# Kernel optimization log

Hardware: AMD Instinct MI355X
Metric: run time of the kernel (lower is better)

Reference implementation:

```python
import jax, jax.numpy as jnp
import numpy as np

B, S, D, H = 8, 1024, 1024, 16
HD = D // H  # head dim 64

def setup_inputs() -> dict:
    key = jax.random.key(0)
    ks = jax.random.split(key, 7)
    def w(k):
        return jax.random.normal(k, (D, D), dtype=jnp.float32) * (1.0 / np.sqrt(D))
    return {
        'q': jax.random.normal(ks[0], (B, S, D), dtype=jnp.float32),
        'k': jax.random.normal(ks[1], (B, S, D), dtype=jnp.float32),
        'v': jax.random.normal(ks[2], (B, S, D), dtype=jnp.float32),
        'Wq': w(ks[3]), 'Wk': w(ks[4]), 'Wv': w(ks[5]), 'Wo': w(ks[6]),
    }

def reference(q, k, v, Wq, Wk, Wv, Wo):
    # projections (nn.Linear, no bias): y = x @ W.T
    def heads(x, W):
        return (x @ W.T).reshape(B, S, H, HD)
    qh, kh, vh = heads(q, Wq), heads(k, Wk), heads(v, Wv)
    scale = 1.0 / np.sqrt(HD).astype(np.float32)
    scores = jnp.einsum('bqhd,bkhd->bhqk', qh, kh) * scale  # [B,H,S,S]
    # masked=True -> causal mask
    causal = jnp.tril(jnp.ones((S, S), dtype=bool))
    scores = jnp.where(causal[None, None], scores, jnp.float32(-1e9))
    attn = jax.nn.softmax(scores, axis=-1)
    out = jnp.einsum('bhqk,bkhd->bqhd', attn, vh).reshape(B, S, D)
    return out @ Wo.T
```

## Files before the change

### kernel.cpp

```cpp
#include <hip/hip_runtime.h>
#include <hip/hip_bf16.h>

#define B_ 8
#define S_ 1024
#define D_ 1024
#define H_ 16
#define HD_ 64
#define M_ (B_*S_)
#define NQB (S_/128)

typedef __attribute__((ext_vector_type(8))) short short8;
typedef __attribute__((ext_vector_type(4))) short short4v;
typedef __attribute__((ext_vector_type(4))) float f32x4;
typedef __attribute__((ext_vector_type(16))) float f32x16;
typedef __attribute__((ext_vector_type(4))) int int4v;
typedef __attribute__((ext_vector_type(2))) int int2v;

#define CSC 0.18033688f

__device__ __forceinline__ unsigned short f2bf(float f) {
    unsigned int u = __float_as_uint(f);
    u += 0x7FFF + ((u >> 16) & 1);
    return (unsigned short)(u >> 16);
}

__device__ __forceinline__ void gload16(const void* g, void* l) {
    __builtin_amdgcn_global_load_lds(
        (const __attribute__((address_space(1))) void*)g,
        (__attribute__((address_space(3))) void*)l, 16, 0, 0);
}

__device__ __forceinline__ int2v plswap(int a, int b) {
    return __builtin_amdgcn_permlane32_swap(a, b, false, false);
}

__device__ __forceinline__ float max3f(float a, float b, float c) {
    return fmaxf(fmaxf(a, b), c);
}

struct CvtSeg { const float* src; unsigned short* dst; };
struct CvtArgs { CvtSeg s[4]; };

__global__ __launch_bounds__(256)
void cvt_w(CvtArgs a)
{
    const CvtSeg seg = a.s[blockIdx.y];
    int i = blockIdx.x * 256 + threadIdx.x;
    float4 x = reinterpret_cast<const float4*>(seg.src)[i*2];
    float4 y = reinterpret_cast<const float4*>(seg.src)[i*2+1];
    short8 v = short8{(short)f2bf(x.x),(short)f2bf(x.y),(short)f2bf(x.z),(short)f2bf(x.w),
                      (short)f2bf(y.x),(short)f2bf(y.y),(short)f2bf(y.z),(short)f2bf(y.w)};
    reinterpret_cast<short8*>(seg.dst)[i] = v;
}

__device__ __forceinline__ void gemm_core_f32A(
    const float* __restrict__ A, const unsigned short* __restrict__ Wb,
    short* lds, int m0, int n0, int tid, f32x4 (&acc)[4][4])
{
    const int K = D_;
    const int lane = tid & 63, wave = tid >> 6;
    const int wr = wave >> 1, wc = wave & 1;
    const int r16 = lane & 15, g4 = lane >> 4;
    const int sr8  = lane >> 3;
    const int slot = lane & 7;
    const int scol = ((lane ^ sr8) & 7) * 8;
    const int wsl  = (slot ^ sr8) << 3;

    float4 ar0[4][2], ar1[4][2];

    #define STAGEB(t, bi)                                                     \
        { _Pragma("unroll")                                                   \
          for (int c = 0; c < 4; ++c) {                                       \
              int chunk = wave*4 + c;                                         \
              gload16(Wb + (size_t)(n0 + chunk*8 + sr8) * K + (t)*64 + scol,  \
                      lds + (bi)*16384 + 8192 + chunk*512);                   \
          } }

    #define LOADA_S(t, AR)                                                    \
        { _Pragma("unroll")                                                   \
          for (int c = 0; c < 4; ++c) {                                       \
              const float* src = A + (size_t)(m0 + wave*32 + c*8 + sr8)*K     \
                                   + (t)*64 + slot*8;                         \
              AR[c][0] = *reinterpret_cast<const float4*>(src);               \
              AR[c][1] = *reinterpret_cast<const float4*>(src + 4);           \
          } }

    #define WRITEA_S(bi, AR)                                                  \
        { _Pragma("unroll")                                                   \
          for (int c = 0; c < 4; ++c) {                                       \
              unsigned w0, w1, w2, w3;                                        \
              asm("v_cvt_pk_bf16_f32 %0, %1, %2" : "=v"(w0) : "v"(AR[c][0].x), "v"(AR[c][0].y)); \
              asm("v_cvt_pk_bf16_f32 %0, %1, %2" : "=v"(w1) : "v"(AR[c][0].z), "v"(AR[c][0].w)); \
              asm("v_cvt_pk_bf16_f32 %0, %1, %2" : "=v"(w2) : "v"(AR[c][1].x), "v"(AR[c][1].y)); \
              asm("v_cvt_pk_bf16_f32 %0, %1, %2" : "=v"(w3) : "v"(AR[c][1].z), "v"(AR[c][1].w)); \
              int4v wi; wi.x = (int)w0; wi.y = (int)w1; wi.z = (int)w2; wi.w = (int)w3; \
              *reinterpret_cast<int4v*>(                                      \
                  &lds[(bi)*16384 + (wave*32 + c*8 + sr8)*64 + wsl]) = wi;    \
          } }

    const int NT = K / 64;

    STAGEB(0, 0);
    LOADA_S(0, ar0);
    asm volatile("s_waitcnt vmcnt(0)" ::: "memory");
    WRITEA_S(0, ar0);
    LOADA_S(1, ar1);
    asm volatile("s_waitcnt lgkmcnt(0)" ::: "memory");
    __builtin_amdgcn_s_barrier();

    #define ITER(t, cur, ARCUR, AROTH)                                        \
    {                                                                         \
        if ((t) + 1 < NT) STAGEB((t)+1, (cur)^1);                             \
        if ((t) + 2 < NT) LOADA_S((t)+2, ARCUR);                              \
        const short* Ab = lds + (cur)*16384;                                  \
        const short* Bb = Ab + 8192;                                          \
        _Pragma("unroll")                                                     \
        for (int ks = 0; ks < 2; ++ks) {                                      \
            short8 af[4], bf[4];                                              \
            _Pragma("unroll")                                                 \
            for (int m = 0; m < 4; ++m) {                                     \
                int r = wr*64 + m*16 + r16;                                   \
                af[m] = *reinterpret_cast<const short8*>(                     \
                    &Ab[r*64 + (((ks*4 + g4) ^ (r16 & 7)) << 3)]);            \
            }                                                                 \
            _Pragma("unroll")                                                 \
            for (int n = 0; n < 4; ++n) {                                     \
                int r = wc*64 + n*16 + r16;                                   \
                bf[n] = *reinterpret_cast<const short8*>(                     \
                    &Bb[r*64 + (((ks*4 + g4) ^ (r16 & 7)) << 3)]);            \
            }                                                                 \
            __builtin_amdgcn_s_setprio(1);                                    \
            _Pragma("unroll")                                                 \
            for (int m = 0; m < 4; ++m)                                       \
                _Pragma("unroll")                                             \
                for (int n = 0; n < 4; ++n)                                   \
                    acc[m][n] = __builtin_amdgcn_mfma_f32_16x16x32_bf16(af[m], bf[n], acc[m][n], 0, 0, 0); \
            __builtin_amdgcn_s_setprio(0);                                    \
        }                                                                     \
        if ((t) + 1 < NT) {                                                   \
            if ((t) + 2 < NT) asm volatile("s_waitcnt vmcnt(8)" ::: "memory");\
            else              asm volatile("s_waitcnt vmcnt(0)" ::: "memory");\
            WRITEA_S((cur)^1, AROTH);                                         \
            asm volatile("s_waitcnt lgkmcnt(0)" ::: "memory");                \
        }                                                                     \
        __builtin_amdgcn_s_barrier();                                         \
    }

    for (int t = 0; t < NT; t += 2) {
        ITER(t,     0, ar0, ar1);
        ITER(t + 1, 1, ar1, ar0);
    }
    #undef ITER
    #undef STAGEB
    #undef LOADA_S
    #undef WRITEA_S
}

__device__ __forceinline__ void gemm_core_bf16A(
    const unsigned short* __restrict__ A, const unsigned short* __restrict__ Wb,
    short* lds, int m0, int n0, int tid, f32x4 (&acc)[4][4])
{
    const int K = D_;
    const int lane = tid & 63, wave = tid >> 6;
    const int wr = wave >> 1, wc = wave & 1;
    const int r16 = lane & 15, g4 = lane >> 4;
    const int srow = lane >> 3;
    const int scol = ((lane ^ srow) & 7) * 8;

    #define STAGE(t, bi)                                                      \
        { _Pragma("unroll")                                                   \
          for (int c = 0; c < 4; ++c) {                                       \
              int chunk = wave*4 + c;                                         \
              gload16(Wb + (size_t)(n0 + chunk*8 + srow) * K + (t)*64 + scol, \
                      lds + (bi)*16384 + 8192 + chunk*512);                   \
              gload16(A + (size_t)(m0 + chunk*8 + srow) * K + (t)*64 + scol,  \
                      lds + (bi)*16384 + chunk*512);                          \
          } }

    STAGE(0, 0);

    const int NT = K / 64;
    for (int t = 0; t < NT; ++t) {
        const int cur = t & 1;
        if (t + 1 < NT) {
            STAGE(t+1, cur^1);
            asm volatile("s_waitcnt vmcnt(8)" ::: "memory");
        } else {
            asm volatile("s_waitcnt vmcnt(0)" ::: "memory");
        }
        __builtin_amdgcn_s_barrier();

        const short* Ab = lds + cur*16384;
        const short* Bb = Ab + 8192;
        #pragma unroll
        for (int ks = 0; ks < 2; ++ks) {
            short8 af[4], bf[4];
            #pragma unroll
            for (int m = 0; m < 4; ++m) {
                int r = wr*64 + m*16 + r16;
                af[m] = *reinterpret_cast<const short8*>(
                    &Ab[r*64 + (((ks*4 + g4) ^ (r16 & 7)) << 3)]);
            }
            #pragma unroll
            for (int n = 0; n < 4; ++n) {
                int r = wc*64 + n*16 + r16;
                bf[n] = *reinterpret_cast<const short8*>(
                    &Bb[r*64 + (((ks*4 + g4) ^ (r16 & 7)) << 3)]);
            }
            __builtin_amdgcn_s_setprio(1);
            #pragma unroll
            for (int m = 0; m < 4; ++m)
                #pragma unroll
                for (int n = 0; n < 4; ++n)
                    acc[m][n] = __builtin_amdgcn_mfma_f32_16x16x32_bf16(af[m], bf[n], acc[m][n], 0, 0, 0);
            __builtin_amdgcn_s_setprio(0);
        }
        __builtin_amdgcn_s_barrier();
    }
    #undef STAGE
}

template<int MODE>
__device__ __forceinline__ void epilogue_vec(
    float* Cl, void* __restrict__ Ov, int m0, int n0, int tid, f32x4 (&acc)[4][4])
{
    const int N = D_;
    const int lane = tid & 63, wave = tid >> 6;
    const int wr = wave >> 1, wc = wave & 1;
    const int r16 = lane & 15, g4 = lane >> 4;

    #pragma unroll
    for (int p = 0; p < 2; ++p) {
        if (p) __syncthreads();
        if (wr == p) {
            #pragma unroll
            for (int m = 0; m < 4; ++m)
                #pragma unroll
                for (int n = 0; n < 4; ++n)
                    #pragma unroll
                    for (int i = 0; i < 4; ++i)
                        Cl[(m*16 + g4*4 + i)*132 + wc*64 + n*16 + r16] = acc[m][n][i];
        }
        __syncthreads();
        if (MODE == 1) {
            #pragma unroll
            for (int j = 0; j < 8; ++j) {
                int c = j*256 + tid;
                int row = c >> 5, cg = c & 31;
                float4 val = *reinterpret_cast<const float4*>(&Cl[row*132 + cg*4]);
                *reinterpret_cast<float4*>(
                    &((float*)Ov)[(size_t)(m0 + p*64 + row)*N + n0 + cg*4]) = val;
            }
        } else {
            #pragma unroll
            for (int j = 0; j < 4; ++j) {
                int c2 = j*256 + tid;
                int row = c2 >> 4, col = (c2 & 15)*8;
                float4 a = *reinterpret_cast<const float4*>(&Cl[row*132 + col]);
                float4 bq = *reinterpret_cast<const float4*>(&Cl[row*132 + col + 4]);
                if (MODE == 3) {
                    a.x *= CSC; a.y *= CSC; a.z *= CSC; a.w *= CSC;
                    bq.x *= CSC; bq.y *= CSC; bq.z *= CSC; bq.w *= CSC;
                }
                short8 v = short8{(short)f2bf(a.x),(short)f2bf(a.y),(short)f2bf(a.z),(short)f2bf(a.w),
                                  (short)f2bf(bq.x),(short)f2bf(bq.y),(short)f2bf(bq.z),(short)f2bf(bq.w)};
                *reinterpret_cast<short8*>(
                    &((unsigned short*)Ov)[(size_t)(m0 + p*64 + row)*N + n0 + col]) = v;
            }
        }
    }
}

struct ProjArgs {
    const float* A[3];
    const unsigned short* W[3];
    void* O[3];
};

__global__ __launch_bounds__(256)
void gemm_proj(ProjArgs pa)
{
    __shared__ __align__(16) short lds[32768];

    const int L = blockIdx.x;
    const int which = L >> 9;
    const int inner = L & 511;
    const int xcd = inner & 7, jj = inner >> 3;
    const int m0 = (xcd*8 + (jj >> 3)) * 128;
    const int n0 = (jj & 7) * 128;
    const int tid = threadIdx.x;

    f32x4 acc[4][4] = {};
    gemm_core_f32A(pa.A[which], pa.W[which], lds, m0, n0, tid, acc);

    if (which == 2) {
        const int lane = tid & 63, wave = tid >> 6;
        const int wr = wave >> 1, wc = wave & 1;
        const int r16 = lane & 15, g4 = lane >> 4;
        #pragma unroll
        for (int m = 0; m < 4; ++m) {
            int row0 = m0 + wr*64 + m*16 + g4*4;
            #pragma unroll
            for (int n = 0; n < 4; ++n) {
                int col = n0 + wc*64 + n*16 + r16;
                size_t vrow = (size_t)((row0 >> 10)*16 + (col >> 6))*64 + (col & 63);
                short4v pk = short4v{(short)f2bf(acc[m][n][0]), (short)f2bf(acc[m][n][1]),
                                     (short)f2bf(acc[m][n][2]), (short)f2bf(acc[m][n][3])};
                *reinterpret_cast<short4v*>((unsigned short*)pa.O[2] + vrow*S_ + (row0 & 1023)) = pk;
            }
        }
    } else if (which == 0) {
        epilogue_vec<3>((float*)lds, pa.O[0], m0, n0, tid, acc);
    } else {
        epilogue_vec<0>((float*)lds, pa.O[1], m0, n0, tid, acc);
    }
}

__global__ __launch_bounds__(256)
void gemm_final(const unsigned short* __restrict__ A, const unsigned short* __restrict__ Wb,
                float* __restrict__ Ov)
{
    __shared__ __align__(16) short lds[32768];

    const int L = blockIdx.x;
    const int xcd = L & 7, jj = L >> 3;
    const int m0 = (xcd*8 + (jj >> 3)) * 128;
    const int n0 = (jj & 7) * 128;
    const int tid = threadIdx.x;

    f32x4 acc[4][4] = {};
    gemm_core_bf16A(A, Wb, lds, m0, n0, tid, acc);
    epilogue_vec<1>((float*)lds, Ov, m0, n0, tid, acc);
}

__global__ __launch_bounds__(256)
void attn_fwd(const unsigned short* __restrict__ Qh,
              const unsigned short* __restrict__ Kh,
              const unsigned short* __restrict__ VtG,
              unsigned short* __restrict__ AO)
{
    __shared__ __align__(16) short Kl[2][64*64];
    __shared__ __align__(16) short Vl[2][64*64];

    const int tid  = threadIdx.x;
    const int lane = tid & 63, wave = tid >> 6;
    const int l31 = lane & 31, h32 = lane >> 5;
    const int L = blockIdx.x;
    const int xcd = L & 7, jj = L >> 3;
    const int pr = jj & 3;
    const int hb = xcd*16 + (jj >> 2);
    const int h = hb & 15, b = hb >> 4;

    const int slot = tid & 7;
    const int r0 = tid >> 3, r1 = r0 + 32;
    const int koff0 = r0*64 + ((slot ^ (r0 & 7)) << 3);
    const int koff1 = r1*64 + ((slot ^ (r1 & 7)) << 3);

    const unsigned short* Kg0 = Kh + ((size_t)b*S_)*D_ + h*HD_;
    const unsigned short* Vg0 = VtG + ((size_t)(b*H_ + h)*HD_)*S_;

    for (int t = 0; t < 2; ++t) {
        const int qb = t ? pr : (NQB - 1 - pr);
        const int q0w = qb*128 + wave*32;
        const int qi  = q0w + l31;

        short8 qf[4];
        #pragma unroll
        for (int m = 0; m < 4; ++m)
            qf[m] = *reinterpret_cast<const short8*>(
                Qh + ((size_t)b*S_ + qi)*D_ + h*HD_ + m*16 + h32*8);

        f32x16 o0 = {}, o1 = {};
        float mrow = -1e30f, lsum = 0.f;
        const int nkb = 2*qb + 2;

        short8 ka, kc, va, vc;
        ka = *reinterpret_cast<const short8*>(Kg0 + (size_t)r0*D_ + slot*8);
        kc = *reinterpret_cast<const short8*>(Kg0 + (size_t)r1*D_ + slot*8);
        va = *reinterpret_cast<const short8*>(Vg0 + (size_t)r0*S_ + slot*8);
        vc = *reinterpret_cast<const short8*>(Vg0 + (size_t)r1*S_ + slot*8);
        *reinterpret_cast<short8*>(&Kl[0][koff0]) = ka;
        *reinterpret_cast<short8*>(&Kl[0][koff1]) = kc;
        *reinterpret_cast<short8*>(&Vl[0][koff0]) = va;
        *reinterpret_cast<short8*>(&Vl[0][koff1]) = vc;
        __syncthreads();

        for (int kb = 0; kb < nkb; ++kb) {
            const int cur = kb & 1;
            const bool havenext = (kb + 1 < nkb);
            if (havenext) {
                const unsigned short* Kg = Kg0 + (size_t)(kb+1)*64*D_;
                const unsigned short* Vg = Vg0 + (kb+1)*64;
                ka = *reinterpret_cast<const short8*>(Kg + (size_t)r0*D_ + slot*8);
                kc = *reinterpret_cast<const short8*>(Kg + (size_t)r1*D_ + slot*8);
                va = *reinterpret_cast<const short8*>(Vg + (size_t)r0*S_ + slot*8);
                vc = *reinterpret_cast<const short8*>(Vg + (size_t)r1*S_ + slot*8);
            }

            if (kb*64 <= q0w + 31) {
                f32x16 p0 = {}, p1 = {};
                __builtin_amdgcn_s_setprio(1);
                #pragma unroll
                for (int m = 0; m < 4; ++m) {
                    short8 kf0 = *reinterpret_cast<const short8*>(
                        &Kl[cur][l31*64 + ((((m<<1)|h32) ^ (l31 & 7)) << 3)]);
                    short8 kf1 = *reinterpret_cast<const short8*>(
                        &Kl[cur][(32 + l31)*64 + ((((m<<1)|h32) ^ (l31 & 7)) << 3)]);
                    p0 = __builtin_amdgcn_mfma_f32_32x32x16_bf16(kf0, qf[m], p0, 0, 0, 0);
                    p1 = __builtin_amdgcn_mfma_f32_32x32x16_bf16(kf1, qf[m], p1, 0, 0, 0);
                }
                __builtin_amdgcn_s_setprio(0);

                if (kb*64 + 63 > q0w) {
                    #pragma unroll
                    for (int r = 0; r < 16; ++r) {
                        int kk = (r & 3) + ((r >> 2) << 3) + (h32 << 2);
                        if (kb*64      + kk > qi) p0[r] = -1e30f;
                        if (kb*64 + 32 + kk > qi) p1[r] = -1e30f;
                    }
                }

                float t0 = max3f(p0[0],  p0[1],  p0[2]);
                float t1 = max3f(p0[3],  p0[4],  p0[5]);
                float t2 = max3f(p0[6],  p0[7],  p0[8]);
                float t3 = max3f(p0[9],  p0[10], p0[11]);
                float t4 = max3f(p0[12], p0[13], p0[14]);
                float t5 = max3f(p0[15], p1[0],  p1[1]);
                float t6 = max3f(p1[2],  p1[3],  p1[4]);
                float t7 = max3f(p1[5],  p1[6],  p1[7]);
                float t8 = max3f(p1[8],  p1[9],  p1[10]);
                float t9 = max3f(p1[11], p1[12], p1[13]);
                float ta = fmaxf(p1[14], p1[15]);
                float mloc = fmaxf(max3f(max3f(t0,t1,t2), max3f(t3,t4,t5), max3f(t6,t7,t8)),
                                   fmaxf(t9, ta));
                int2v mm = plswap(__float_as_int(mloc), __float_as_int(mloc));
                float pm = fmaxf(__int_as_float(mm.x), __int_as_float(mm.y));

                if (__any(pm > mrow + 11.5416f)) {
                    float mn = fmaxf(mrow, pm);
                    float so = exp2f(mrow - mn);
                    #pragma unroll
                    for (int r = 0; r < 16; ++r) { o0[r] *= so; o1[r] *= so; }
                    lsum *= so;
                    mrow = mn;
                }

                #pragma unroll
                for (int r = 0; r < 16; ++r) p0[r] = exp2f(p0[r] - mrow);
                #pragma unroll
                for (int r = 0; r < 16; ++r) p1[r] = exp2f(p1[r] - mrow);
                float sq[8];
                #pragma unroll
                for (int r = 0; r < 8; ++r)
                    sq[r] = (p0[2*r] + p0[2*r+1]) + (p1[2*r] + p1[2*r+1]);
                float rs = ((sq[0]+sq[1]) + (sq[2]+sq[3])) + ((sq[4]+sq[5]) + (sq[6]+sq[7]));
                int2v ss = plswap(__float_as_int(rs), __float_as_int(rs));
                lsum += __int_as_float(ss.x) + __int_as_float(ss.y);

                #pragma unroll
                for (int m = 0; m < 4; ++m) {
                    const int mb = (m & 1) * 8;
                    unsigned int C0, C1, C2, C3;
                    if (m < 2) {
                        asm("v_cvt_pk_bf16_f32 %0, %1, %2" : "=v"(C0) : "v"(p0[mb+0]), "v"(p0[mb+1]));
                        asm("v_cvt_pk_bf16_f32 %0, %1, %2" : "=v"(C1) : "v"(p0[mb+2]), "v"(p0[mb+3]));
                        asm("v_cvt_pk_bf16_f32 %0, %1, %2" : "=v"(C2) : "v"(p0[mb+4]), "v"(p0[mb+5]));
                        asm("v_cvt_pk_bf16_f32 %0, %1, %2" : "=v"(C3) : "v"(p0[mb+6]), "v"(p0[mb+7]));
                    } else {
                        asm("v_cvt_pk_bf16_f32 %0, %1, %2" : "=v"(C0) : "v"(p1[mb+0]), "v"(p1[mb+1]));
                        asm("v_cvt_pk_bf16_f32 %0, %1, %2" : "=v"(C1) : "v"(p1[mb+2]), "v"(p1[mb+3]));
                        asm("v_cvt_pk_bf16_f32 %0, %1, %2" : "=v"(C2) : "v"(p1[mb+4]), "v"(p1[mb+5]));
                        asm("v_cvt_pk_bf16_f32 %0, %1, %2" : "=v"(C3) : "v"(p1[mb+6]), "v"(p1[mb+7]));
                    }
                    int2v s0 = plswap((int)C0, (int)C2);
                    int2v s1 = plswap((int)C1, (int)C3);
                    int4v wi; wi.x = s0.x; wi.y = s1.x; wi.z = s0.y; wi.w = s1.y;
                    short8 pf = __builtin_bit_cast(short8, wi);

                    short8 vf0 = *reinterpret_cast<const short8*>(
                        &Vl[cur][l31*64 + ((((m<<1)|h32) ^ (l31 & 7)) << 3)]);
                    short8 vf1 = *reinterpret_cast<const short8*>(
                        &Vl[cur][(32 + l31)*64 + ((((m<<1)|h32) ^ (l31 & 7)) << 3)]);
                    o0 = __builtin_amdgcn_mfma_f32_32x32x16_bf16(vf0, pf, o0, 0, 0, 0);
                    o1 = __builtin_amdgcn_mfma_f32_32x32x16_bf16(vf1, pf, o1, 0, 0, 0);
                }
            }

            if (havenext) {
                const int nb = cur ^ 1;
                *reinterpret_cast<short8*>(&Kl[nb][koff0]) = ka;
                *reinterpret_cast<short8*>(&Kl[nb][koff1]) = kc;
                *reinterpret_cast<short8*>(&Vl[nb][koff0]) = va;
                *reinterpret_cast<short8*>(&Vl[nb][koff1]) = vc;
            }
            __syncthreads();
        }

        float inv = 1.f / lsum;
        #pragma unroll
        for (int tt = 0; tt < 2; ++tt) {
            #pragma unroll
            for (int g = 0; g < 4; ++g) {
                short4v pk;
                #pragma unroll
                for (int j = 0; j < 4; ++j) {
                    float val = (tt ? o1[g*4+j] : o0[g*4+j]) * inv;
                    pk[j] = (short)f2bf(val);
                }
                int d = tt*32 + g*8 + h32*4;
                *reinterpret_cast<short4v*>(AO + ((size_t)b*S_ + qi)*D_ + h*HD_ + d) = pk;
            }
        }
    }
}

extern "C" void kernel_launch(void* const* d_in, const int* in_sizes, int n_in,
                              void* d_out, int out_size, void* d_ws, size_t ws_size,
                              hipStream_t stream) {
    const float* q  = (const float*)d_in[0];
    const float* k  = (const float*)d_in[1];
    const float* v  = (const float*)d_in[2];
    const float* Wq = (const float*)d_in[3];
    const float* Wk = (const float*)d_in[4];
    const float* Wv = (const float*)d_in[5];
    const float* Wo = (const float*)d_in[6];

    unsigned short* Wqb = (unsigned short*)d_ws;
    unsigned short* Wkb = Wqb + (size_t)D_*D_;
    unsigned short* Wvb = Wkb + (size_t)D_*D_;
    unsigned short* Wob = Wvb + (size_t)D_*D_;
    unsigned short* Qh  = Wob + (size_t)D_*D_;
    unsigned short* Kh  = Qh  + (size_t)M_*D_;
    unsigned short* VtG = Kh  + (size_t)M_*D_;
    unsigned short* AO  = VtG + (size_t)M_*D_;

    dim3 blk(256);
    CvtArgs ca;
    ca.s[0] = CvtSeg{Wq, Wqb};
    ca.s[1] = CvtSeg{Wk, Wkb};
    ca.s[2] = CvtSeg{Wv, Wvb};
    ca.s[3] = CvtSeg{Wo, Wob};
    cvt_w<<<dim3(512, 4), blk, 0, stream>>>(ca);

    ProjArgs pa;
    pa.A[0] = q;  pa.W[0] = Wqb; pa.O[0] = Qh;
    pa.A[1] = k;  pa.W[1] = Wkb; pa.O[1] = Kh;
    pa.A[2] = v;  pa.W[2] = Wvb; pa.O[2] = VtG;
    gemm_proj<<<dim3(1536), blk, 0, stream>>>(pa);

    attn_fwd<<<dim3(512), blk, 0, stream>>>(Qh, Kh, VtG, AO);

    gemm_final<<<dim3(512), blk, 0, stream>>>(AO, Wob, (float*)d_out);
}
```

Measured before the change: 151.5 us.

## Stage 128-key K/V tiles via direct global-to-LDS loads in attention

The attention loop now processes 128 keys per iteration as two 64-key halves, with double-buffered LDS holding 128-row K and V tiles. The tiles are filled by asynchronous global-to-LDS loads (gload16). The XOR swizzle moves to the global source column, so the LDS destinations stay linear. This halves the number of barrier and stage cycles, removes the register round trip for staging, and issues both QK^T MMA groups back to back before softmax. In exchange, LDS per block doubles to 64KB, which may cut occupancy. An explicit vmcnt(0) wait before each barrier also limits how much load latency is hidden.

```diff
diff --git a/kernel.cpp b/kernel.cpp
--- a/kernel.cpp
+++ b/kernel.cpp
@@ -339,8 +339,8 @@
               const unsigned short* __restrict__ VtG,
               unsigned short* __restrict__ AO)
 {
-    __shared__ __align__(16) short Kl[2][64*64];
-    __shared__ __align__(16) short Vl[2][64*64];
+    __shared__ __align__(16) short Kl[2][2][64*64];
+    __shared__ __align__(16) short Vl[2][2][64*64];
 
     const int tid  = threadIdx.x;
     const int lane = tid & 63, wave = tid >> 6;
@@ -353,11 +353,108 @@
 
     const int slot = tid & 7;
     const int r0 = tid >> 3, r1 = r0 + 32;
-    const int koff0 = r0*64 + ((slot ^ (r0 & 7)) << 3);
-    const int koff1 = r1*64 + ((slot ^ (r1 & 7)) << 3);
+    const int sc8 = ((slot ^ (r0 & 7)) << 3);
 
     const unsigned short* Kg0 = Kh + ((size_t)b*S_)*D_ + h*HD_;
     const unsigned short* Vg0 = VtG + ((size_t)(b*H_ + h)*HD_)*S_;
+
+    #define STAGEKV128(j1, nb)                                                \
+        { const unsigned short* Kg = Kg0 + (size_t)(j1)*128*D_;               \
+          const unsigned short* Vg = Vg0 + (size_t)(j1)*128;                  \
+          gload16(Kg + (size_t)r0*D_ + sc8,      &Kl[nb][0][r0*64 + slot*8]); \
+          gload16(Kg + (size_t)r1*D_ + sc8,      &Kl[nb][0][r1*64 + slot*8]); \
+          gload16(Kg + (size_t)(r0+64)*D_ + sc8, &Kl[nb][1][r0*64 + slot*8]); \
+          gload16(Kg + (size_t)(r1+64)*D_ + sc8, &Kl[nb][1][r1*64 + slot*8]); \
+          gload16(Vg + (size_t)r0*S_ + sc8,      &Vl[nb][0][r0*64 + slot*8]); \
+          gload16(Vg + (size_t)r1*S_ + sc8,      &Vl[nb][0][r1*64 + slot*8]); \
+          gload16(Vg + 64 + (size_t)r0*S_ + sc8, &Vl[nb][1][r0*64 + slot*8]); \
+          gload16(Vg + 64 + (size_t)r1*S_ + sc8, &Vl[nb][1][r1*64 + slot*8]); }
+
+    #define QKT_W(cur, vw, p0, p1)                                            \
+        { __builtin_amdgcn_s_setprio(1);                                      \
+          _Pragma("unroll")                                                   \
+          for (int m = 0; m < 4; ++m) {                                       \
+              short8 kf0 = *reinterpret_cast<const short8*>(                  \
+                  &Kl[cur][vw][l31*64 + ((((m<<1)|h32) ^ (l31 & 7)) << 3)]);  \
+              short8 kf1 = *reinterpret_cast<const short8*>(                  \
+                  &Kl[cur][vw][(32 + l31)*64 + ((((m<<1)|h32) ^ (l31 & 7)) << 3)]); \
+              p0 = __builtin_amdgcn_mfma_f32_32x32x16_bf16(kf0, qf[m], p0, 0, 0, 0); \
+              p1 = __builtin_amdgcn_mfma_f32_32x32x16_bf16(kf1, qf[m], p1, 0, 0, 0); \
+          }                                                                   \
+          __builtin_amdgcn_s_setprio(0); }
+
+    #define MASK_W(kb, p0, p1)                                                \
+        if ((kb)*64 + 63 > q0w) {                                             \
+            _Pragma("unroll")                                                 \
+            for (int r = 0; r < 16; ++r) {                                    \
+                int kk = (r & 3) + ((r >> 2) << 3) + (h32 << 2);              \
+                if ((kb)*64      + kk > qi) p0[r] = -1e30f;                   \
+                if ((kb)*64 + 32 + kk > qi) p1[r] = -1e30f;                   \
+            } }
+
+    #define SOFTMAX_W(p0, p1) {                                               \
+        float t0 = max3f(p0[0],  p0[1],  p0[2]);                              \
+        float t1 = max3f(p0[3],  p0[4],  p0[5]);                              \
+        float t2 = max3f(p0[6],  p0[7],  p0[8]);                              \
+        float t3 = max3f(p0[9],  p0[10], p0[11]);                             \
+        float t4 = max3f(p0[12], p0[13], p0[14]);                             \
+        float t5 = max3f(p0[15], p1[0],  p1[1]);                              \
+        float t6 = max3f(p1[2],  p1[3],  p1[4]);                              \
+        float t7 = max3f(p1[5],  p1[6],  p1[7]);                              \
+        float t8 = max3f(p1[8],  p1[9],  p1[10]);                             \
+        float t9 = max3f(p1[11], p1[12], p1[13]);                             \
+        float ta = fmaxf(p1[14], p1[15]);                                     \
+        float mloc = fmaxf(max3f(max3f(t0,t1,t2), max3f(t3,t4,t5),            \
+                                 max3f(t6,t7,t8)), fmaxf(t9, ta));            \
+        int2v mm = plswap(__float_as_int(mloc), __float_as_int(mloc));        \
+        float pm = fmaxf(__int_as_float(mm.x), __int_as_float(mm.y));         \
+        if (__any(pm > mrow + 11.5416f)) {                                    \
+            float mn = fmaxf(mrow, pm);                                       \
+            float so = exp2f(mrow - mn);                                      \
+            _Pragma("unroll")                                                 \
+            for (int r = 0; r < 16; ++r) { o0[r] *= so; o1[r] *= so; }        \
+            lsum *= so;                                                       \
+            mrow = mn;                                                        \
+        }                                                                     \
+        _Pragma("unroll")                                                     \
+        for (int r = 0; r < 16; ++r) p0[r] = exp2f(p0[r] - mrow);             \
+        _Pragma("unroll")                                                     \
+        for (int r = 0; r < 16; ++r) p1[r] = exp2f(p1[r] - mrow);             \
+        float sq[8];                                                          \
+        _Pragma("unroll")                                                     \
+        for (int r = 0; r < 8; ++r)                                           \
+            sq[r] = (p0[2*r] + p0[2*r+1]) + (p1[2*r] + p1[2*r+1]);            \
+        float rs = ((sq[0]+sq[1]) + (sq[2]+sq[3])) + ((sq[4]+sq[5]) + (sq[6]+sq[7])); \
+        int2v ss = plswap(__float_as_int(rs), __float_as_int(rs));            \
+        lsum += __int_as_float(ss.x) + __int_as_float(ss.y); }
+
+    #define PV_W(cur, vw, p0, p1)                                             \
+        { _Pragma("unroll")                                                   \
+          for (int m = 0; m < 4; ++m) {                                       \
+              const int mb = (m & 1) * 8;                                     \
+              unsigned int C0, C1, C2, C3;                                    \
+              if (m < 2) {                                                    \
+                  asm("v_cvt_pk_bf16_f32 %0, %1, %2" : "=v"(C0) : "v"(p0[mb+0]), "v"(p0[mb+1])); \
+                  asm("v_cvt_pk_bf16_f32 %0, %1, %2" : "=v"(C1) : "v"(p0[mb+2]), "v"(p0[mb+3])); \
+                  asm("v_cvt_pk_bf16_f32 %0, %1, %2" : "=v"(C2) : "v"(p0[mb+4]), "v"(p0[mb+5])); \
+                  asm("v_cvt_pk_bf16_f32 %0, %1, %2" : "=v"(C3) : "v"(p0[mb+6]), "v"(p0[mb+7])); \
+              } else {                                                        \
+                  asm("v_cvt_pk_bf16_f32 %0, %1, %2" : "=v"(C0) : "v"(p1[mb+0]), "v"(p1[mb+1])); \
+                  asm("v_cvt_pk_bf16_f32 %0, %1, %2" : "=v"(C1) : "v"(p1[mb+2]), "v"(p1[mb+3])); \
+                  asm("v_cvt_pk_bf16_f32 %0, %1, %2" : "=v"(C2) : "v"(p1[mb+4]), "v"(p1[mb+5])); \
+                  asm("v_cvt_pk_bf16_f32 %0, %1, %2" : "=v"(C3) : "v"(p1[mb+6]), "v"(p1[mb+7])); \
+              }                                                               \
+              int2v s0 = plswap((int)C0, (int)C2);                            \
+              int2v s1 = plswap((int)C1, (int)C3);                            \
+              int4v wi; wi.x = s0.x; wi.y = s1.x; wi.z = s0.y; wi.w = s1.y;   \
+              short8 pf = __builtin_bit_cast(short8, wi);                     \
+              short8 vf0 = *reinterpret_cast<const short8*>(                  \
+                  &Vl[cur][vw][l31*64 + ((((m<<1)|h32) ^ (l31 & 7)) << 3)]);  \
+              short8 vf1 = *reinterpret_cast<const short8*>(                  \
+                  &Vl[cur][vw][(32 + l31)*64 + ((((m<<1)|h32) ^ (l31 & 7)) << 3)]); \
+              o0 = __builtin_amdgcn_mfma_f32_32x32x16_bf16(vf0, pf, o0, 0, 0, 0); \
+              o1 = __builtin_amdgcn_mfma_f32_32x32x16_bf16(vf1, pf, o1, 0, 0, 0); \
+          } }
 
     for (int t = 0; t < 2; ++t) {
         const int qb = t ? pr : (NQB - 1 - pr);
@@ -372,127 +469,34 @@
 
         f32x16 o0 = {}, o1 = {};
         float mrow = -1e30f, lsum = 0.f;
-        const int nkb = 2*qb + 2;
-
-        short8 ka, kc, va, vc;
-        ka = *reinterpret_cast<const short8*>(Kg0 + (size_t)r0*D_ + slot*8);
-        kc = *reinterpret_cast<const short8*>(Kg0 + (size_t)r1*D_ + slot*8);
-        va = *reinterpret_cast<const short8*>(Vg0 + (size_t)r0*S_ + slot*8);
-        vc = *reinterpret_cast<const short8*>(Vg0 + (size_t)r1*S_ + slot*8);
-        *reinterpret_cast<short8*>(&Kl[0][koff0]) = ka;
-        *reinterpret_cast<short8*>(&Kl[0][koff1]) = kc;
-        *reinterpret_cast<short8*>(&Vl[0][koff0]) = va;
-        *reinterpret_cast<short8*>(&Vl[0][koff1]) = vc;
+        const int np = qb + 1;
+
+        STAGEKV128(0, 0);
+        asm volatile("s_waitcnt vmcnt(0)" ::: "memory");
         __syncthreads();
 
-        for (int kb = 0; kb < nkb; ++kb) {
-            const int cur = kb & 1;
-            const bool havenext = (kb + 1 < nkb);
-            if (havenext) {
-                const unsigned short* Kg = Kg0 + (size_t)(kb+1)*64*D_;
-                const unsigned short* Vg = Vg0 + (kb+1)*64;
-                ka = *reinterpret_cast<const short8*>(Kg + (size_t)r0*D_ + slot*8);
-                kc = *reinterpret_cast<const short8*>(Kg + (size_t)r1*D_ + slot*8);
-                va = *reinterpret_cast<const short8*>(Vg + (size_t)r0*S_ + slot*8);
-                vc = *reinterpret_cast<const short8*>(Vg + (size_t)r1*S_ + slot*8);
-            }
-
-            if (kb*64 <= q0w + 31) {
-                f32x16 p0 = {}, p1 = {};
-                __builtin_amdgcn_s_setprio(1);
-                #pragma unroll
-                for (int m = 0; m < 4; ++m) {
-                    short8 kf0 = *reinterpret_cast<const short8*>(
-                        &Kl[cur][l31*64 + ((((m<<1)|h32) ^ (l31 & 7)) << 3)]);
-                    short8 kf1 = *reinterpret_cast<const short8*>(
-                        &Kl[cur][(32 + l31)*64 + ((((m<<1)|h32) ^ (l31 & 7)) << 3)]);
-                    p0 = __builtin_amdgcn_mfma_f32_32x32x16_bf16(kf0, qf[m], p0, 0, 0, 0);
-                    p1 = __builtin_amdgcn_mfma_f32_32x32x16_bf16(kf1, qf[m], p1, 0, 0, 0);
-                }
-                __builtin_amdgcn_s_setprio(0);
-
-                if (kb*64 + 63 > q0w) {
-                    #pragma unroll
-                    for (int r = 0; r < 16; ++r) {
-                        int kk = (r & 3) + ((r >> 2) << 3) + (h32 << 2);
-                        if (kb*64      + kk > qi) p0[r] = -1e30f;
-                        if (kb*64 + 32 + kk > qi) p1[r] = -1e30f;
-                    }
-                }
-
-                float t0 = max3f(p0[0],  p0[1],  p0[2]);
-                float t1 = max3f(p0[3],  p0[4],  p0[5]);
-                float t2 = max3f(p0[6],  p0[7],  p0[8]);
-                float t3 = max3f(p0[9],  p0[10], p0[11]);
-                float t4 = max3f(p0[12], p0[13], p0[14]);
-                float t5 = max3f(p0[15], p1[0],  p1[1]);
-                float t6 = max3f(p1[2],  p1[3],  p1[4]);
-                float t7 = max3f(p1[5],  p1[6],  p1[7]);
-                float t8 = max3f(p1[8],  p1[9],  p1[10]);
-                float t9 = max3f(p1[11], p1[12], p1[13]);
-                float ta = fmaxf(p1[14], p1[15]);
-                float mloc = fmaxf(max3f(max3f(t0,t1,t2), max3f(t3,t4,t5), max3f(t6,t7,t8)),
-                                   fmaxf(t9, ta));
-                int2v mm = plswap(__float_as_int(mloc), __float_as_int(mloc));
-                float pm = fmaxf(__int_as_float(mm.x), __int_as_float(mm.y));
-
-                if (__any(pm > mrow + 11.5416f)) {
-                    float mn = fmaxf(mrow, pm);
-                    float so = exp2f(mrow - mn);
-                    #pragma unroll
-                    for (int r = 0; r < 16; ++r) { o0[r] *= so; o1[r] *= so; }
-                    lsum *= so;
-                    mrow = mn;
-                }
-
-                #pragma unroll
-                for (int r = 0; r < 16; ++r) p0[r] = exp2f(p0[r] - mrow);
-                #pragma unroll
-                for (int r = 0; r < 16; ++r) p1[r] = exp2f(p1[r] - mrow);
-                float sq[8];
-                #pragma unroll
-                for (int r = 0; r < 8; ++r)
-                    sq[r] = (p0[2*r] + p0[2*r+1]) + (p1[2*r] + p1[2*r+1]);
-                float rs = ((sq[0]+sq[1]) + (sq[2]+sq[3])) + ((sq[4]+sq[5]) + (sq[6]+sq[7]));
-                int2v ss = plswap(__float_as_int(rs), __float_as_int(rs));
-                lsum += __int_as_float(ss.x) + __int_as_float(ss.y);
-
-                #pragma unroll
-                for (int m = 0; m < 4; ++m) {
-                    const int mb = (m & 1) * 8;
-                    unsigned int C0, C1, C2, C3;
-                    if (m < 2) {
-                        asm("v_cvt_pk_bf16_f32 %0, %1, %2" : "=v"(C0) : "v"(p0[mb+0]), "v"(p0[mb+1]));
-                        asm("v_cvt_pk_bf16_f32 %0, %1, %2" : "=v"(C1) : "v"(p0[mb+2]), "v"(p0[mb+3]));
-                        asm("v_cvt_pk_bf16_f32 %0, %1, %2" : "=v"(C2) : "v"(p0[mb+4]), "v"(p0[mb+5]));
-                        asm("v_cvt_pk_bf16_f32 %0, %1, %2" : "=v"(C3) : "v"(p0[mb+6]), "v"(p0[mb+7]));
-                    } else {
-                        asm("v_cvt_pk_bf16_f32 %0, %1, %2" : "=v"(C0) : "v"(p1[mb+0]), "v"(p1[mb+1]));
-                        asm("v_cvt_pk_bf16_f32 %0, %1, %2" : "=v"(C1) : "v"(p1[mb+2]), "v"(p1[mb+3]));
-                        asm("v_cvt_pk_bf16_f32 %0, %1, %2" : "=v"(C2) : "v"(p1[mb+4]), "v"(p1[mb+5]));
-                        asm("v_cvt_pk_bf16_f32 %0, %1, %2" : "=v"(C3) : "v"(p1[mb+6]), "v"(p1[mb+7]));
-                    }
-                    int2v s0 = plswap((int)C0, (int)C2);
-                    int2v s1 = plswap((int)C1, (int)C3);
-                    int4v wi; wi.x = s0.x; wi.y = s1.x; wi.z = s0.y; wi.w = s1.y;
-                    short8 pf = __builtin_bit_cast(short8, wi);
-
-                    short8 vf0 = *reinterpret_cast<const short8*>(
-                        &Vl[cur][l31*64 + ((((m<<1)|h32) ^ (l31 & 7)) << 3)]);
-                    short8 vf1 = *reinterpret_cast<const short8*>(
-                        &Vl[cur][(32 + l31)*64 + ((((m<<1)|h32) ^ (l31 & 7)) << 3)]);
-                    o0 = __builtin_amdgcn_mfma_f32_32x32x16_bf16(vf0, pf, o0, 0, 0, 0);
-                    o1 = __builtin_amdgcn_mfma_f32_32x32x16_bf16(vf1, pf, o1, 0, 0, 0);
-                }
-            }
-
-            if (havenext) {
-                const int nb = cur ^ 1;
-                *reinterpret_cast<short8*>(&Kl[nb][koff0]) = ka;
-                *reinterpret_cast<short8*>(&Kl[nb][koff1]) = kc;
-                *reinterpret_cast<short8*>(&Vl[nb][koff0]) = va;
-                *reinterpret_cast<short8*>(&Vl[nb][koff1]) = vc;
-            }
+        for (int j = 0; j < np; ++j) {
+            const int cur = j & 1;
+            if (j + 1 < np) STAGEKV128(j+1, cur^1);
+
+            const int kbA = 2*j, kbB = 2*j + 1;
+            const bool actB = (kbB*64 <= q0w + 31);
+
+            f32x16 pA0 = {}, pA1 = {}, pB0 = {}, pB1 = {};
+            QKT_W(cur, 0, pA0, pA1);
+            if (actB) QKT_W(cur, 1, pB0, pB1);
+
+            MASK_W(kbA, pA0, pA1);
+            SOFTMAX_W(pA0, pA1);
+            PV_W(cur, 0, pA0, pA1);
+
+            if (actB) {
+                MASK_W(kbB, pB0, pB1);
+                SOFTMAX_W(pB0, pB1);
+                PV_W(cur, 1, pB0, pB1);
+            }
+
+            asm volatile("s_waitcnt vmcnt(0)" ::: "memory");
             __syncthreads();
         }
 
@@ -503,15 +507,20 @@
             for (int g = 0; g < 4; ++g) {
                 short4v pk;
                 #pragma unroll
-                for (int j = 0; j < 4; ++j) {
-                    float val = (tt ? o1[g*4+j] : o0[g*4+j]) * inv;
-                    pk[j] = (short)f2bf(val);
+                for (int j2 = 0; j2 < 4; ++j2) {
+                    float val = (tt ? o1[g*4+j2] : o0[g*4+j2]) * inv;
+                    pk[j2] = (short)f2bf(val);
                 }
                 int d = tt*32 + g*8 + h32*4;
                 *reinterpret_cast<short4v*>(AO + ((size_t)b*S_ + qi)*D_ + h*HD_ + d) = pk;
             }
         }
     }
+    #undef STAGEKV128
+    #undef QKT_W
+    #undef MASK_W
+    #undef SOFTMAX_W
+    #undef PV_W
 }
 
 extern "C" void kernel_launch(void* const* d_in, const int* in_sizes, int n_in,
```

After: 168.1 us. 1.11x slower.
